# Kernel tuning notes

Hardware: AMD Instinct MI355X
Metric: run time of the kernel (lower is better)

Reference implementation:

```python
import jax, jax.numpy as jnp
import numpy as np

H = 4          # attention heads
LEAKY = 0.2    # PyG GATConv default negative_slope
N = 10000
E = 320000
F_IN = 256
F_OUT = 256


def _gat_layer(x, src, dst, W, a_src, a_dst, b):
    """One PyG-style GATConv with heads=H, concat=False (head mean).
    x: [N, in], W: [in, H*out], a_src/a_dst: [H, out], b: [out]."""
    n = x.shape[0]
    out = W.shape[1] // H
    h = (x @ W).reshape(n, H, out)                       # [N,H,out]
    al_s = (h * a_src).sum(-1)                           # [N,H]
    al_d = (h * a_dst).sum(-1)                           # [N,H]
    e = jax.nn.leaky_relu(al_s[src] + al_d[dst], LEAKY)  # [Etot,H]
    # segment softmax over incoming edges of each destination node
    m = jax.ops.segment_max(e, dst, num_segments=n)      # [N,H]
    ex = jnp.exp(e - m[dst])
    s = jax.ops.segment_sum(ex, dst, num_segments=n)     # [N,H]
    alpha = ex / (s[dst] + 1e-16)                        # [Etot,H]
    agg = jax.ops.segment_sum(h[src] * alpha[:, :, None], dst, num_segments=n)  # [N,H,out]
    return agg.mean(axis=1) + b                          # concat=False -> head mean, then bias


def setup_inputs() -> dict:
    key = jax.random.key(0)
    ks = jax.random.split(key, 20)
    inp = {
        "x": jax.random.normal(ks[0], (N, F_IN), dtype=jnp.float32),
        "edge_index": jax.random.randint(ks[1], (2, E), 0, N),
    }
    for l in range(4):
        fin = F_IN if l == 0 else F_OUT
        inp[f"W{l}"] = jax.random.normal(ks[2 + 4 * l], (fin, H * F_OUT), dtype=jnp.float32) * 0.05
        inp[f"as{l}"] = jax.random.normal(ks[3 + 4 * l], (H, F_OUT), dtype=jnp.float32) * 0.05
        inp[f"ad{l}"] = jax.random.normal(ks[4 + 4 * l], (H, F_OUT), dtype=jnp.float32) * 0.05
        inp[f"b{l}"] = jnp.zeros((F_OUT,), dtype=jnp.float32)
    return inp


def reference(x, edge_index, W0, as0, ad0, b0, W1, as1, ad1, b1,
              W2, as2, ad2, b2, W3, as3, ad3, b3):
    n = x.shape[0]
    loop = jnp.arange(n)
    src = jnp.concatenate([edge_index[0], loop])   # add_self_loops=True
    dst = jnp.concatenate([edge_index[1], loop])
    h = jax.nn.relu(_gat_layer(x, src, dst, W0, as0, ad0, b0))
    h = jax.nn.relu(_gat_layer(h, src, dst, W1, as1, ad1, b1))
    h = jax.nn.relu(_gat_layer(h, src, dst, W2, as2, ad2, b2))
    z = jnp.tanh(_gat_layer(h, src, dst, W3, as3, ad3, b3))
    adj_recon = jax.nn.sigmoid(z @ z.T)            # [N,N]
    return adj_recon, z
```

## Files before the change

### kernel.cpp

```cpp
#include <hip/hip_runtime.h>
#include <hip/hip_bf16.h>

#define NNODES 10000
#define NEDGE_IN 320000
#define ETOT (NEDGE_IN + NNODES)
#define FDIM 256
#define NT 79

typedef float floatx4 __attribute__((ext_vector_type(4)));
typedef __bf16 bf16x8 __attribute__((ext_vector_type(8)));

__device__ __forceinline__ float bf2f(unsigned short u) {
  return __uint_as_float((unsigned)u << 16);
}

__global__ void count_deg_kernel(const int* __restrict__ ei, int* __restrict__ counts) {
  int e = blockIdx.x * blockDim.x + threadIdx.x;
  if (e >= ETOT) return;
  int d = (e < NEDGE_IN) ? ei[NEDGE_IN + e] : (e - NEDGE_IN);
  atomicAdd(&counts[d], 1);
}

__global__ __launch_bounds__(256) void scan_kernel(const int* __restrict__ counts,
                                                   int* __restrict__ row_ptr,
                                                   int* __restrict__ fill) {
  int t = threadIdx.x;
  const int CH = 40;
  int base = t * CH;
  int local[CH];
  int sum = 0;
#pragma unroll
  for (int i = 0; i < CH; i++) {
    int idx = base + i;
    int v = (idx < NNODES) ? counts[idx] : 0;
    local[i] = sum;
    sum += v;
  }
  __shared__ int ssum[256];
  ssum[t] = sum;
  __syncthreads();
  for (int off = 1; off < 256; off <<= 1) {
    int add = (t >= off) ? ssum[t - off] : 0;
    __syncthreads();
    ssum[t] += add;
    __syncthreads();
  }
  int excl = ssum[t] - sum;
#pragma unroll
  for (int i = 0; i < CH; i++) {
    int idx = base + i;
    if (idx < NNODES) {
      int v = excl + local[i];
      row_ptr[idx] = v;
      fill[idx] = v;
    }
  }
  if (t == 255) row_ptr[NNODES] = ssum[255];
}

__global__ void scatter_kernel(const int* __restrict__ ei, int* __restrict__ fill,
                               int* __restrict__ col_idx) {
  int e = blockIdx.x * blockDim.x + threadIdx.x;
  if (e >= ETOT) return;
  int s, d;
  if (e < NEDGE_IN) { s = ei[e]; d = ei[NEDGE_IN + e]; } else { s = d = e - NEDGE_IN; }
  int pos = atomicAdd(&fill[d], 1);
  col_idx[pos] = s;
}

__global__ __launch_bounds__(256) void split_bf16_kernel(const float* __restrict__ z,
                                                         unsigned short* __restrict__ hi,
                                                         unsigned short* __restrict__ lo) {
  int i = blockIdx.x * 256 + threadIdx.x;
  if (i >= NNODES * FDIM) return;
  float v = z[i];
  unsigned u = __float_as_uint(v);
  unsigned hu = u & 0xffff0000u;
  float r = v - __uint_as_float(hu);
  hi[i] = (unsigned short)(u >> 16);
  lo[i] = (unsigned short)(__float_as_uint(r) >> 16);
}

__global__ __launch_bounds__(256) void prep_bt_kernel(const float* __restrict__ W,
                                                      unsigned short* __restrict__ btHi,
                                                      unsigned short* __restrict__ btLo) {
  __shared__ float tile[32][33];
  int t = threadIdx.x;
  int tx = t & 31, ty = t >> 5;
  int f0 = blockIdx.x * 32, k0 = blockIdx.y * 32, h = blockIdx.z;
#pragma unroll
  for (int i = 0; i < 4; i++) {
    int kr = ty + 8 * i;
    tile[kr][tx] = W[(size_t)(k0 + kr) * 1024 + h * 256 + f0 + tx];
  }
  __syncthreads();
#pragma unroll
  for (int i = 0; i < 4; i++) {
    int fr = ty + 8 * i;
    float v = 0.25f * tile[tx][fr];
    unsigned u = __float_as_uint(v);
    float r = v - __uint_as_float(u & 0xffff0000u);
    size_t o = (size_t)(f0 + fr) * 1024 + h * 256 + k0 + tx;
    btHi[o] = (unsigned short)(u >> 16);
    btLo[o] = (unsigned short)(__float_as_uint(r) >> 16);
  }
}

__global__ __launch_bounds__(256) void prep_wa_kernel(const float* __restrict__ W,
                                                      const float* __restrict__ a_src,
                                                      const float* __restrict__ a_dst,
                                                      float* __restrict__ Was,
                                                      float* __restrict__ Wad) {
  int k = blockIdx.x, t = threadIdx.x;
  float ps[4], pd[4];
#pragma unroll
  for (int hd = 0; hd < 4; hd++) {
    float w = W[(size_t)k * 1024 + hd * 256 + t];
    ps[hd] = w * a_src[hd * 256 + t];
    pd[hd] = w * a_dst[hd * 256 + t];
  }
  __shared__ float red[8][4];
  int lane = t & 63, wv = t >> 6;
#pragma unroll
  for (int q = 0; q < 8; q++) {
    float v = (q < 4) ? ps[q] : pd[q - 4];
#pragma unroll
    for (int off = 32; off > 0; off >>= 1) v += __shfl_down(v, off, 64);
    if (lane == 0) red[q][wv] = v;
  }
  __syncthreads();
  if (t < 8) {
    float v = red[t][0] + red[t][1] + red[t][2] + red[t][3];
    if (t < 4) Was[k * 4 + t] = v;
    else Wad[k * 4 + (t - 4)] = v;
  }
}

__global__ __launch_bounds__(256) void al_kernel(const float* __restrict__ X,
                                                 const float* __restrict__ Was,
                                                 const float* __restrict__ Wad,
                                                 float* __restrict__ al_s,
                                                 float* __restrict__ al_d) {
  int n = blockIdx.x, t = threadIdx.x;
  float x = X[(size_t)n * 256 + t];
  float4 ws = *reinterpret_cast<const float4*>(Was + t * 4);
  float4 wd = *reinterpret_cast<const float4*>(Wad + t * 4);
  float ps[4] = {x * ws.x, x * ws.y, x * ws.z, x * ws.w};
  float pd[4] = {x * wd.x, x * wd.y, x * wd.z, x * wd.w};
  __shared__ float red[8][4];
  int lane = t & 63, wv = t >> 6;
#pragma unroll
  for (int q = 0; q < 8; q++) {
    float v = (q < 4) ? ps[q] : pd[q - 4];
#pragma unroll
    for (int off = 32; off > 0; off >>= 1) v += __shfl_down(v, off, 64);
    if (lane == 0) red[q][wv] = v;
  }
  __syncthreads();
  if (t < 8) {
    float v = red[t][0] + red[t][1] + red[t][2] + red[t][3];
    if (t < 4) al_s[n * 4 + t] = v;
    else al_d[n * 4 + (t - 4)] = v;
  }
}

__global__ __launch_bounds__(256) void gat_gather_kernel(
    const unsigned short* __restrict__ xhi, const float* __restrict__ al_s,
    const float* __restrict__ al_d, const int* __restrict__ row_ptr,
    const int* __restrict__ col_idx,
    unsigned short* __restrict__ aggHi, unsigned short* __restrict__ aggLo) {
  int t = threadIdx.x;
  int lane = t & 63, wv = t >> 6;
  int n = blockIdx.x * 4 + wv;
  int start = row_ptr[n], end = row_ptr[n + 1];
  float4 ald4 = *reinterpret_cast<const float4*>(al_d + n * 4);
  float ald[4] = {ald4.x, ald4.y, ald4.z, ald4.w};

  float acc[4][4] = {};
  float esum[4] = {0.f, 0.f, 0.f, 0.f};

  for (int c = start; c < end; c += 64) {
    int nch = min(64, end - c);
    int s = 0;
    float ex[4] = {0.f, 0.f, 0.f, 0.f};
    if (lane < nch) {
      s = col_idx[c + lane];
      float4 as4 = *reinterpret_cast<const float4*>(al_s + s * 4);
      float lv[4] = {as4.x + ald[0], as4.y + ald[1], as4.z + ald[2], as4.w + ald[3]};
#pragma unroll
      for (int h = 0; h < 4; h++) {
        float l = lv[h];
        l = (l > 0.f) ? l : 0.2f * l;
        l = fminf(l, 60.f);
        float e = __expf(l);
        ex[h] = e;
        esum[h] += e;
      }
    }
    for (int i = 0; i < nch; i++) {
      int si = __shfl(s, i, 64);
      float e0 = __shfl(ex[0], i, 64);
      float e1 = __shfl(ex[1], i, 64);
      float e2 = __shfl(ex[2], i, 64);
      float e3 = __shfl(ex[3], i, 64);
      ushort4 xv = *reinterpret_cast<const ushort4*>(xhi + (size_t)si * 256 + lane * 4);
      float xf0 = bf2f(xv.x), xf1 = bf2f(xv.y), xf2 = bf2f(xv.z), xf3 = bf2f(xv.w);
      acc[0][0] += xf0 * e0; acc[0][1] += xf1 * e0; acc[0][2] += xf2 * e0; acc[0][3] += xf3 * e0;
      acc[1][0] += xf0 * e1; acc[1][1] += xf1 * e1; acc[1][2] += xf2 * e1; acc[1][3] += xf3 * e1;
      acc[2][0] += xf0 * e2; acc[2][1] += xf1 * e2; acc[2][2] += xf2 * e2; acc[2][3] += xf3 * e2;
      acc[3][0] += xf0 * e3; acc[3][1] += xf1 * e3; acc[3][2] += xf2 * e3; acc[3][3] += xf3 * e3;
    }
  }

#pragma unroll
  for (int h = 0; h < 4; h++) {
#pragma unroll
    for (int m = 32; m > 0; m >>= 1) esum[h] += __shfl_xor(esum[h], m, 64);
  }

#pragma unroll
  for (int h = 0; h < 4; h++) {
    float inv = 1.f / (esum[h] + 1e-16f);
    ushort4 hv, lv;
    unsigned short* hp = (unsigned short*)&hv;
    unsigned short* lp = (unsigned short*)&lv;
#pragma unroll
    for (int j = 0; j < 4; j++) {
      float v = acc[h][j] * inv;
      unsigned u = __float_as_uint(v);
      float r = v - __uint_as_float(u & 0xffff0000u);
      hp[j] = (unsigned short)(u >> 16);
      lp[j] = (unsigned short)(__float_as_uint(r) >> 16);
    }
    size_t o = (size_t)n * 1024 + h * 256 + lane * 4;
    *reinterpret_cast<ushort4*>(aggHi + o) = hv;
    *reinterpret_cast<ushort4*>(aggLo + o) = lv;
  }
}

#define AHI_OFF 0
#define ALO_OFF 16384
#define BHI_OFF 32768
#define BLO_OFF 49152

__global__ __launch_bounds__(256, 2) void gemm_out_kernel(
    const unsigned short* __restrict__ aggHi, const unsigned short* __restrict__ aggLo,
    const unsigned short* __restrict__ btHi, const unsigned short* __restrict__ btLo,
    const float* __restrict__ bias, float* __restrict__ outF,
    unsigned short* __restrict__ outHi, unsigned short* __restrict__ outLo, int act_tanh) {
  __shared__ __align__(16) char lds[65536];
  int t = threadIdx.x;
  int lane = t & 63, wv = t >> 6;
  int quad = lane >> 4, lr = lane & 15;
  int row0 = blockIdx.y * 128;
  int col0 = blockIdx.x * 128;
  int wm = (wv & 1) * 64, wn = (wv >> 1) * 64;

  floatx4 acc[4][4];
#pragma unroll
  for (int i = 0; i < 4; i++)
#pragma unroll
    for (int j = 0; j < 4; j++) acc[i][j] = (floatx4){0.f, 0.f, 0.f, 0.f};

  for (int ks = 0; ks < 16; ks++) {
#pragma unroll
    for (int mat = 0; mat < 4; mat++) {
      const unsigned short* src = (mat == 0) ? aggHi : (mat == 1) ? aggLo : (mat == 2) ? btHi : btLo;
      int rowbase = (mat < 2) ? row0 : col0;
      int maxrow = (mat < 2) ? (NNODES - 1) : 255;
      int ldsoff = mat * 16384;
#pragma unroll
      for (int it = 0; it < 4; it++) {
        int lin = ((wv * 4 + it) << 10) + lane * 16;
        int R = lin >> 7;
        int c = (lin >> 4) & 7;
        int g = c ^ (R & 7);
        int gr = rowbase + R;
        if (gr > maxrow) gr = maxrow;
        const char* gp = (const char*)src + (size_t)gr * 2048 + ks * 128 + g * 16;
        __builtin_amdgcn_global_load_lds(
            (const __attribute__((address_space(1))) void*)gp,
            (__attribute__((address_space(3))) void*)(lds + ldsoff + lin), 16, 0, 0);
      }
    }
    __syncthreads();

#pragma unroll
    for (int ksub = 0; ksub < 2; ksub++) {
      int g = ksub * 4 + quad;
      bf16x8 ah[4], al_[4], bh[4], bl[4];
#pragma unroll
      for (int mi = 0; mi < 4; mi++) {
        int m = wm + mi * 16 + lr;
        int off = m * 128 + ((g ^ (m & 7)) << 4);
        ah[mi] = *(const bf16x8*)(lds + AHI_OFF + off);
        al_[mi] = *(const bf16x8*)(lds + ALO_OFF + off);
      }
#pragma unroll
      for (int ni = 0; ni < 4; ni++) {
        int n = wn + ni * 16 + lr;
        int off = n * 128 + ((g ^ (n & 7)) << 4);
        bh[ni] = *(const bf16x8*)(lds + BHI_OFF + off);
        bl[ni] = *(const bf16x8*)(lds + BLO_OFF + off);
      }
#pragma unroll
      for (int mi = 0; mi < 4; mi++)
#pragma unroll
        for (int ni = 0; ni < 4; ni++) {
          acc[mi][ni] = __builtin_amdgcn_mfma_f32_16x16x32_bf16(ah[mi], bh[ni], acc[mi][ni], 0, 0, 0);
          acc[mi][ni] = __builtin_amdgcn_mfma_f32_16x16x32_bf16(ah[mi], bl[ni], acc[mi][ni], 0, 0, 0);
          acc[mi][ni] = __builtin_amdgcn_mfma_f32_16x16x32_bf16(al_[mi], bh[ni], acc[mi][ni], 0, 0, 0);
        }
    }
    __syncthreads();
  }

#pragma unroll
  for (int mi = 0; mi < 4; mi++) {
#pragma unroll
    for (int ni = 0; ni < 4; ni++) {
      int col = col0 + wn + ni * 16 + lr;
      float bv = bias[col];
#pragma unroll
      for (int r = 0; r < 4; r++) {
        int row = row0 + wm + mi * 16 + quad * 4 + r;
        if (row < NNODES) {
          float v = acc[mi][ni][r] + bv;
          v = act_tanh ? tanhf(v) : fmaxf(v, 0.f);
          size_t o = (size_t)row * 256 + col;
          outF[o] = v;
          unsigned u = __float_as_uint(v);
          float rr = v - __uint_as_float(u & 0xffff0000u);
          outHi[o] = (unsigned short)(u >> 16);
          outLo[o] = (unsigned short)(__float_as_uint(rr) >> 16);
        }
      }
    }
  }
}

__global__ __launch_bounds__(256, 2) void zzt_mfma_kernel(
    const unsigned short* __restrict__ zhi, const unsigned short* __restrict__ zlo,
    float* __restrict__ out) {
  __shared__ __align__(16) char lds[65536];
  int t = threadIdx.x;
  int lane = t & 63, wv = t >> 6;
  int quad = lane >> 4, lr = lane & 15;

  int p = blockIdx.x;
  int bi = (int)((159.0f - sqrtf(159.0f * 159.0f - 8.0f * (float)p)) * 0.5f);
  if (bi < 0) bi = 0;
  if (bi > NT - 1) bi = NT - 1;
  while (bi * NT - bi * (bi - 1) / 2 > p) bi--;
  while ((bi + 1) * NT - (bi + 1) * bi / 2 <= p) bi++;
  int bj = bi + (p - (bi * NT - bi * (bi - 1) / 2));
  int row0 = bi * 128;
  int col0 = bj * 128;
  int wm = (wv & 1) * 64, wn = (wv >> 1) * 64;

  floatx4 acc[4][4];
#pragma unroll
  for (int i = 0; i < 4; i++)
#pragma unroll
    for (int j = 0; j < 4; j++) acc[i][j] = (floatx4){0.f, 0.f, 0.f, 0.f};

  for (int ks = 0; ks < 4; ks++) {
#pragma unroll
    for (int mat = 0; mat < 4; mat++) {
      const unsigned short* src = (mat == 0 || mat == 2) ? zhi : zlo;
      int rowbase = (mat < 2) ? row0 : col0;
      int ldsoff = mat * 16384;
#pragma unroll
      for (int it = 0; it < 4; it++) {
        int lin = ((wv * 4 + it) << 10) + lane * 16;
        int R = lin >> 7;
        int c = (lin >> 4) & 7;
        int g = c ^ (R & 7);
        int gr = rowbase + R;
        if (gr > NNODES - 1) gr = NNODES - 1;
        const char* gp = (const char*)src + (size_t)gr * 512 + ks * 128 + g * 16;
        __builtin_amdgcn_global_load_lds(
            (const __attribute__((address_space(1))) void*)gp,
            (__attribute__((address_space(3))) void*)(lds + ldsoff + lin), 16, 0, 0);
      }
    }
    __syncthreads();

#pragma unroll
    for (int ksub = 0; ksub < 2; ksub++) {
      int g = ksub * 4 + quad;
      bf16x8 ah[4], al_[4], bh[4], bl[4];
#pragma unroll
      for (int mi = 0; mi < 4; mi++) {
        int m = wm + mi * 16 + lr;
        int off = m * 128 + ((g ^ (m & 7)) << 4);
        ah[mi] = *(const bf16x8*)(lds + AHI_OFF + off);
        al_[mi] = *(const bf16x8*)(lds + ALO_OFF + off);
      }
#pragma unroll
      for (int ni = 0; ni < 4; ni++) {
        int n = wn + ni * 16 + lr;
        int off = n * 128 + ((g ^ (n & 7)) << 4);
        bh[ni] = *(const bf16x8*)(lds + BHI_OFF + off);
        bl[ni] = *(const bf16x8*)(lds + BLO_OFF + off);
      }
#pragma unroll
      for (int mi = 0; mi < 4; mi++)
#pragma unroll
        for (int ni = 0; ni < 4; ni++) {
          acc[mi][ni] = __builtin_amdgcn_mfma_f32_16x16x32_bf16(ah[mi], bh[ni], acc[mi][ni], 0, 0, 0);
          acc[mi][ni] = __builtin_amdgcn_mfma_f32_16x16x32_bf16(ah[mi], bl[ni], acc[mi][ni], 0, 0, 0);
          acc[mi][ni] = __builtin_amdgcn_mfma_f32_16x16x32_bf16(al_[mi], bh[ni], acc[mi][ni], 0, 0, 0);
        }
    }
    __syncthreads();
  }

  bool diag = (bi == bj);
#pragma unroll
  for (int mi = 0; mi < 4; mi++) {
#pragma unroll
    for (int ni = 0; ni < 4; ni++) {
      int col = col0 + wn + ni * 16 + lr;
      if (col >= NNODES) continue;
      float4 sv;
      sv.x = 1.f / (1.f + __expf(-acc[mi][ni][0]));
      sv.y = 1.f / (1.f + __expf(-acc[mi][ni][1]));
      sv.z = 1.f / (1.f + __expf(-acc[mi][ni][2]));
      sv.w = 1.f / (1.f + __expf(-acc[mi][ni][3]));
      float svv[4] = {sv.x, sv.y, sv.z, sv.w};
      int r0 = row0 + wm + mi * 16 + quad * 4;
#pragma unroll
      for (int r = 0; r < 4; r++) {
        if (r0 + r < NNODES) out[(size_t)(r0 + r) * NNODES + col] = svv[r];
      }
      if (!diag) {
        if (r0 + 3 < NNODES) {
          *reinterpret_cast<float4*>(&out[(size_t)col * NNODES + r0]) = sv;
        } else {
#pragma unroll
          for (int r = 0; r < 4; r++)
            if (r0 + r < NNODES) out[(size_t)col * NNODES + r0 + r] = svv[r];
        }
      }
    }
  }
}

extern "C" void kernel_launch(void* const* d_in, const int* in_sizes, int n_in,
                              void* d_out, int out_size, void* d_ws, size_t ws_size,
                              hipStream_t stream) {
  const float* x = (const float*)d_in[0];
  const int* ei = (const int*)d_in[1];
  const float* W[4]  = {(const float*)d_in[2], (const float*)d_in[6], (const float*)d_in[10], (const float*)d_in[14]};
  const float* as[4] = {(const float*)d_in[3], (const float*)d_in[7], (const float*)d_in[11], (const float*)d_in[15]};
  const float* ad[4] = {(const float*)d_in[4], (const float*)d_in[8], (const float*)d_in[12], (const float*)d_in[16]};
  const float* bs[4] = {(const float*)d_in[5], (const float*)d_in[9], (const float*)d_in[13], (const float*)d_in[17]};

  char* ws = (char*)d_ws;
  size_t off = 0;
  auto alloc = [&](size_t bytes) -> void* {
    void* p = ws + off;
    off = (off + bytes + 255) & ~(size_t)255;
    return p;
  };
  unsigned short* aggHi = (unsigned short*)alloc(sizeof(unsigned short) * (size_t)NNODES * 1024);
  unsigned short* aggLo = (unsigned short*)alloc(sizeof(unsigned short) * (size_t)NNODES * 1024);
  unsigned short* shi   = (unsigned short*)alloc(sizeof(unsigned short) * (size_t)NNODES * FDIM);
  unsigned short* slo   = (unsigned short*)alloc(sizeof(unsigned short) * (size_t)NNODES * FDIM);
  unsigned short* btHi  = (unsigned short*)alloc(sizeof(unsigned short) * 256 * 1024);
  unsigned short* btLo  = (unsigned short*)alloc(sizeof(unsigned short) * 256 * 1024);
  float* xF    = (float*)alloc(sizeof(float) * (size_t)NNODES * FDIM);
  float* al_s  = (float*)alloc(sizeof(float) * NNODES * 4);
  float* al_d  = (float*)alloc(sizeof(float) * NNODES * 4);
  float* Was   = (float*)alloc(sizeof(float) * 256 * 4);
  float* Wad   = (float*)alloc(sizeof(float) * 256 * 4);
  int* counts  = (int*)alloc(sizeof(int) * NNODES);
  int* row_ptr = (int*)alloc(sizeof(int) * (NNODES + 1));
  int* fill    = (int*)alloc(sizeof(int) * NNODES);
  int* col_idx = (int*)alloc(sizeof(int) * ETOT);

  hipMemsetAsync(counts, 0, sizeof(int) * NNODES, stream);
  int eblocks = (ETOT + 255) / 256;
  count_deg_kernel<<<eblocks, 256, 0, stream>>>(ei, counts);
  scan_kernel<<<1, 256, 0, stream>>>(counts, row_ptr, fill);
  scatter_kernel<<<eblocks, 256, 0, stream>>>(ei, fill, col_idx);
  split_bf16_kernel<<<(NNODES * FDIM + 255) / 256, 256, 0, stream>>>(x, shi, slo);

  float* z = (float*)d_out + (size_t)NNODES * NNODES;
  const float* xin = x;
  for (int l = 0; l < 4; l++) {
    prep_bt_kernel<<<dim3(8, 8, 4), 256, 0, stream>>>(W[l], btHi, btLo);
    prep_wa_kernel<<<256, 256, 0, stream>>>(W[l], as[l], ad[l], Was, Wad);
    al_kernel<<<NNODES, 256, 0, stream>>>(xin, Was, Wad, al_s, al_d);
    gat_gather_kernel<<<NNODES / 4, 256, 0, stream>>>(shi, al_s, al_d, row_ptr, col_idx,
                                                      aggHi, aggLo);
    float* outF = (l == 3) ? z : xF;
    gemm_out_kernel<<<dim3(2, 79), 256, 0, stream>>>(aggHi, aggLo, btHi, btLo, bs[l],
                                                     outF, shi, slo, l == 3 ? 1 : 0);
    xin = xF;
  }
  zzt_mfma_kernel<<<NT * (NT + 1) / 2, 256, 0, stream>>>(shi, slo, (float*)d_out);
}
```

Before: 1.061 ms.

## Stage ZZT transpose stores via LDS, unroll gather, drop fp32 activation buffer

The mirrored (transposed) writes of the sigmoid(ZZ^T) tile now go through an LDS tile with a rotated layout, so each column row is written as contiguous float4 runs instead of scattered strided float4 stores. The gather kernel keeps edge indices and weights in shared memory and unrolls the neighbor loop by four, so several independent row loads are in flight at once. The intermediate fp32 activation buffer is removed and al_kernel rebuilds x from the bf16 hi/lo split, which cuts one write and one read per layer. The cost is extra LDS traffic and a block barrier in the ZZT epilogue, plus a slight precision change in the attention logits.

```diff
diff --git a/kernel.cpp b/kernel.cpp
--- a/kernel.cpp
+++ b/kernel.cpp
@@ -136,13 +136,14 @@
   }
 }
 
-__global__ __launch_bounds__(256) void al_kernel(const float* __restrict__ X,
+__global__ __launch_bounds__(256) void al_kernel(const unsigned short* __restrict__ xhi,
+                                                 const unsigned short* __restrict__ xlo,
                                                  const float* __restrict__ Was,
                                                  const float* __restrict__ Wad,
                                                  float* __restrict__ al_s,
                                                  float* __restrict__ al_d) {
   int n = blockIdx.x, t = threadIdx.x;
-  float x = X[(size_t)n * 256 + t];
+  float x = bf2f(xhi[(size_t)n * 256 + t]) + bf2f(xlo[(size_t)n * 256 + t]);
   float4 ws = *reinterpret_cast<const float4*>(Was + t * 4);
   float4 wd = *reinterpret_cast<const float4*>(Wad + t * 4);
   float ps[4] = {x * ws.x, x * ws.y, x * ws.z, x * ws.w};
@@ -164,11 +165,22 @@
   }
 }
 
+#define ACC4(xv, e)                                                              \
+  {                                                                              \
+    float f0 = bf2f(xv.x), f1 = bf2f(xv.y), f2 = bf2f(xv.z), f3 = bf2f(xv.w);    \
+    acc[0][0] += f0 * e.x; acc[0][1] += f1 * e.x; acc[0][2] += f2 * e.x; acc[0][3] += f3 * e.x; \
+    acc[1][0] += f0 * e.y; acc[1][1] += f1 * e.y; acc[1][2] += f2 * e.y; acc[1][3] += f3 * e.y; \
+    acc[2][0] += f0 * e.z; acc[2][1] += f1 * e.z; acc[2][2] += f2 * e.z; acc[2][3] += f3 * e.z; \
+    acc[3][0] += f0 * e.w; acc[3][1] += f1 * e.w; acc[3][2] += f2 * e.w; acc[3][3] += f3 * e.w; \
+  }
+
 __global__ __launch_bounds__(256) void gat_gather_kernel(
     const unsigned short* __restrict__ xhi, const float* __restrict__ al_s,
     const float* __restrict__ al_d, const int* __restrict__ row_ptr,
     const int* __restrict__ col_idx,
     unsigned short* __restrict__ aggHi, unsigned short* __restrict__ aggLo) {
+  __shared__ int sS[4][64];
+  __shared__ float4 sE[4][64];
   int t = threadIdx.x;
   int lane = t & 63, wv = t >> 6;
   int n = blockIdx.x * 4 + wv;
@@ -197,19 +209,29 @@
         esum[h] += e;
       }
     }
-    for (int i = 0; i < nch; i++) {
-      int si = __shfl(s, i, 64);
-      float e0 = __shfl(ex[0], i, 64);
-      float e1 = __shfl(ex[1], i, 64);
-      float e2 = __shfl(ex[2], i, 64);
-      float e3 = __shfl(ex[3], i, 64);
-      ushort4 xv = *reinterpret_cast<const ushort4*>(xhi + (size_t)si * 256 + lane * 4);
-      float xf0 = bf2f(xv.x), xf1 = bf2f(xv.y), xf2 = bf2f(xv.z), xf3 = bf2f(xv.w);
-      acc[0][0] += xf0 * e0; acc[0][1] += xf1 * e0; acc[0][2] += xf2 * e0; acc[0][3] += xf3 * e0;
-      acc[1][0] += xf0 * e1; acc[1][1] += xf1 * e1; acc[1][2] += xf2 * e1; acc[1][3] += xf3 * e1;
-      acc[2][0] += xf0 * e2; acc[2][1] += xf1 * e2; acc[2][2] += xf2 * e2; acc[2][3] += xf3 * e2;
-      acc[3][0] += xf0 * e3; acc[3][1] += xf1 * e3; acc[3][2] += xf2 * e3; acc[3][3] += xf3 * e3;
-    }
+    sS[wv][lane] = s;
+    sE[wv][lane] = make_float4(ex[0], ex[1], ex[2], ex[3]);
+    __asm__ __volatile__("" ::: "memory");
+    int i = 0;
+    for (; i + 4 <= nch; i += 4) {
+      int s0 = sS[wv][i], s1 = sS[wv][i + 1], s2 = sS[wv][i + 2], s3 = sS[wv][i + 3];
+      float4 e0 = sE[wv][i], e1 = sE[wv][i + 1], e2 = sE[wv][i + 2], e3 = sE[wv][i + 3];
+      ushort4 x0 = *reinterpret_cast<const ushort4*>(xhi + (size_t)s0 * 256 + lane * 4);
+      ushort4 x1 = *reinterpret_cast<const ushort4*>(xhi + (size_t)s1 * 256 + lane * 4);
+      ushort4 x2 = *reinterpret_cast<const ushort4*>(xhi + (size_t)s2 * 256 + lane * 4);
+      ushort4 x3 = *reinterpret_cast<const ushort4*>(xhi + (size_t)s3 * 256 + lane * 4);
+      ACC4(x0, e0);
+      ACC4(x1, e1);
+      ACC4(x2, e2);
+      ACC4(x3, e3);
+    }
+    for (; i < nch; i++) {
+      int s0 = sS[wv][i];
+      float4 e0 = sE[wv][i];
+      ushort4 x0 = *reinterpret_cast<const ushort4*>(xhi + (size_t)s0 * 256 + lane * 4);
+      ACC4(x0, e0);
+    }
+    __asm__ __volatile__("" ::: "memory");
   }
 
 #pragma unroll
@@ -328,7 +350,7 @@
           float v = acc[mi][ni][r] + bv;
           v = act_tanh ? tanhf(v) : fmaxf(v, 0.f);
           size_t o = (size_t)row * 256 + col;
-          outF[o] = v;
+          if (outF) outF[o] = v;
           unsigned u = __float_as_uint(v);
           float rr = v - __uint_as_float(u & 0xffff0000u);
           outHi[o] = (unsigned short)(u >> 16);
@@ -417,31 +439,45 @@
   }
 
   bool diag = (bi == bj);
+  float4* ltile = (float4*)lds;
+
 #pragma unroll
   for (int mi = 0; mi < 4; mi++) {
 #pragma unroll
     for (int ni = 0; ni < 4; ni++) {
-      int col = col0 + wn + ni * 16 + lr;
-      if (col >= NNODES) continue;
+      int cl = wn + ni * 16 + lr;
+      int col = col0 + cl;
       float4 sv;
       sv.x = 1.f / (1.f + __expf(-acc[mi][ni][0]));
       sv.y = 1.f / (1.f + __expf(-acc[mi][ni][1]));
       sv.z = 1.f / (1.f + __expf(-acc[mi][ni][2]));
       sv.w = 1.f / (1.f + __expf(-acc[mi][ni][3]));
       float svv[4] = {sv.x, sv.y, sv.z, sv.w};
-      int r0 = row0 + wm + mi * 16 + quad * 4;
-#pragma unroll
-      for (int r = 0; r < 4; r++) {
-        if (r0 + r < NNODES) out[(size_t)(r0 + r) * NNODES + col] = svv[r];
+      int rl0 = wm + mi * 16 + quad * 4;
+      if (col < NNODES) {
+#pragma unroll
+        for (int r = 0; r < 4; r++) {
+          int row = row0 + rl0 + r;
+          if (row < NNODES) out[(size_t)row * NNODES + col] = svv[r];
+        }
       }
       if (!diag) {
-        if (r0 + 3 < NNODES) {
-          *reinterpret_cast<float4*>(&out[(size_t)col * NNODES + r0]) = sv;
-        } else {
-#pragma unroll
-          for (int r = 0; r < 4; r++)
-            if (r0 + r < NNODES) out[(size_t)col * NNODES + r0 + r] = svv[r];
-        }
+        int rq = rl0 >> 2;
+        ltile[cl * 32 + ((rq + cl) & 31)] = sv;
+      }
+    }
+  }
+
+  if (!diag) {
+    __syncthreads();
+#pragma unroll
+    for (int it = 0; it < 16; it++) {
+      int cl = wv * 32 + it * 2 + (lane >> 5);
+      int rq = lane & 31;
+      int col = col0 + cl;
+      if (col < NNODES) {
+        float4 v = ltile[cl * 32 + ((rq + cl) & 31)];
+        *reinterpret_cast<float4*>(&out[(size_t)col * NNODES + row0 + 4 * rq]) = v;
       }
     }
   }
@@ -470,7 +506,6 @@
   unsigned short* slo   = (unsigned short*)alloc(sizeof(unsigned short) * (size_t)NNODES * FDIM);
   unsigned short* btHi  = (unsigned short*)alloc(sizeof(unsigned short) * 256 * 1024);
   unsigned short* btLo  = (unsigned short*)alloc(sizeof(unsigned short) * 256 * 1024);
-  float* xF    = (float*)alloc(sizeof(float) * (size_t)NNODES * FDIM);
   float* al_s  = (float*)alloc(sizeof(float) * NNODES * 4);
   float* al_d  = (float*)alloc(sizeof(float) * NNODES * 4);
   float* Was   = (float*)alloc(sizeof(float) * 256 * 4);
@@ -488,17 +523,15 @@
   split_bf16_kernel<<<(NNODES * FDIM + 255) / 256, 256, 0, stream>>>(x, shi, slo);
 
   float* z = (float*)d_out + (size_t)NNODES * NNODES;
-  const float* xin = x;
   for (int l = 0; l < 4; l++) {
     prep_bt_kernel<<<dim3(8, 8, 4), 256, 0, stream>>>(W[l], btHi, btLo);
     prep_wa_kernel<<<256, 256, 0, stream>>>(W[l], as[l], ad[l], Was, Wad);
-    al_kernel<<<NNODES, 256, 0, stream>>>(xin, Was, Wad, al_s, al_d);
+    al_kernel<<<NNODES, 256, 0, stream>>>(shi, slo, Was, Wad, al_s, al_d);
     gat_gather_kernel<<<NNODES / 4, 256, 0, stream>>>(shi, al_s, al_d, row_ptr, col_idx,
                                                       aggHi, aggLo);
-    float* outF = (l == 3) ? z : xF;
+    float* outF = (l == 3) ? z : (float*)nullptr;
     gemm_out_kernel<<<dim3(2, 79), 256, 0, stream>>>(aggHi, aggLo, btHi, btLo, bs[l],
                                                      outF, shi, slo, l == 3 ? 1 : 0);
-    xin = xF;
   }
   zzt_mfma_kernel<<<NT * (NT + 1) / 2, 256, 0, stream>>>(shi, slo, (float*)d_out);
 }
```

Result: faster. 996.4 us (-6.1%).
